# Performance work log

Measured on AMD Instinct MI355X. Metric: run time of the kernel, lower is better.

Reference implementation:

```python
import jax, jax.numpy as jnp
import numpy as np

RADIUS = 0.2
NSAMPLE = 32


def setup_inputs() -> dict:
    key = jax.random.key(0)
    k1, k2 = jax.random.split(key)
    B, N = 8, 4096
    xyz = jax.random.uniform(k1, (B, N, 3), dtype=jnp.float32)
    xyz_new = jax.random.uniform(k2, (B, N, 3), dtype=jnp.float32)  # ignored by forward, kept for signature fidelity
    return {"xyz": xyz, "xyz_new": xyz_new}


def _ball_query(radius, nsample, xyz, new_xyz):
    # xyz: [B, N, 3] source points; new_xyz: [B, M, 3] query centers.
    # Returns idx: [B, M, nsample] int32, matching pointnet2 CUDA ball_query:
    # first `nsample` indices j (in increasing j order) with ||q - p_j||^2 < r^2;
    # unused slots are filled with the first valid index.
    B, N, _ = xyz.shape
    sq_src = jnp.sum(xyz * xyz, axis=-1)          # [B, N]
    sq_q = jnp.sum(new_xyz * new_xyz, axis=-1)    # [B, M]
    # d2[b, m, n] = ||q_m - p_n||^2
    d2 = sq_q[:, :, None] + sq_src[:, None, :] - 2.0 * jnp.einsum(
        "bmc,bnc->bmn", new_xyz, xyz)             # [B, M, N]
    mask = d2 < (radius * radius)                 # [B, M, N] bool
    # key = index j when within radius, else sentinel N (sorts to the end)
    idx_range = jnp.arange(N, dtype=jnp.int32)
    keys = jnp.where(mask, idx_range[None, None, :], jnp.int32(N))
    sorted_keys = jnp.sort(keys, axis=-1)[..., :nsample]  # [B, M, nsample]
    first = sorted_keys[..., 0:1]                 # first valid index (pad value)
    idx = jnp.where(sorted_keys < N, sorted_keys, first)
    return idx.astype(jnp.int32)


def reference(xyz, xyz_new):
    # Faithful to the module: ball_query(radius, nsample, xyz, xyz) — xyz_new unused.
    return _ball_query(RADIUS, NSAMPLE, xyz, xyz)
```

## Files before the change

### kernel.cpp

```cpp
#include <hip/hip_runtime.h>
#include <cstdint>


#define BQ_N   4096
#define BQ_B   8
#define BQ_NS  32
#define BQ_R2  0.04f

__device__ __forceinline__ float sq_plain(float x, float y, float z) {
    float r, t;
    asm("v_mul_f32 %0, %2, %2\n\t"
        "v_mul_f32 %1, %3, %3\n\t"
        "v_add_f32 %0, %0, %1\n\t"
        "v_mul_f32 %1, %4, %4\n\t"
        "v_add_f32 %0, %0, %1"
        : "=&v"(r), "=&v"(t)
        : "v"(x), "v"(y), "v"(z));
    return r;
}

__device__ __forceinline__ float d2_mixed(float qx, float qy, float qz, float sqq,
                                          float sx, float sy, float sz, float sqs) {
    float r, t;
    asm("v_mul_f32 %0, %2, %5\n\t"
        "v_fma_f32 %0, %3, %6, %0\n\t"
        "v_fma_f32 %0, %4, %7, %0\n\t"
        "v_add_f32 %0, %0, %0\n\t"
        "v_add_f32 %1, %8, %9\n\t"
        "v_sub_f32 %0, %1, %0"
        : "=&v"(r), "=&v"(t)
        : "v"(qx), "v"(qy), "v"(qz), "v"(sx), "v"(sy), "v"(sz),
          "v"(sqq), "v"(sqs));
    return r;
}

__device__ __forceinline__ void emit_query(int* orow, int lane, uint64_t word) {
    const int cnt = __popcll(word);
    int incl = cnt;
    #pragma unroll
    for (int off = 1; off < 64; off <<= 1) {
        const int t = __shfl_up(incl, off);
        if (lane >= off) incl += t;
    }
    const int pre   = incl - cnt;
    const int total = __shfl(incl, 63);

    int first;
    const uint64_t nz = __ballot(word != 0ull);
    if (nz == 0ull) {
        first = BQ_N;
    } else {
        const int fl = __builtin_ctzll(nz);
        const uint64_t fw = __shfl(word, fl);
        first = (fl << 6) + __builtin_ctzll(fw);
    }

    uint64_t w = word;
    int pos = pre;
    while (w != 0ull && pos < BQ_NS) {
        const int bit = __builtin_ctzll(w);
        orow[pos] = (lane << 6) + bit;
        w &= (w - 1);
        ++pos;
    }
    if (lane >= total && lane < BQ_NS) orow[lane] = first;
}

__global__ __launch_bounds__(512, 4)
void ball_query_kernel(const float* __restrict__ xyz, int* __restrict__ out)
{
    __shared__ float4 pts[BQ_N];

    const int b     = blockIdx.x >> 6;
    const int qbase = (blockIdx.x & 63) << 6;
    const float* __restrict__ src = xyz + (size_t)b * BQ_N * 3;
    const int lane = threadIdx.x & 63;
    const int wid  = threadIdx.x >> 6;
    int* __restrict__ outb = out + (size_t)(b * BQ_N) * BQ_NS;

    for (int j = threadIdx.x; j < BQ_N; j += 512) {
        const float x = src[3 * j + 0];
        const float y = src[3 * j + 1];
        const float z = src[3 * j + 2];
        pts[j] = make_float4(x, y, z, sq_plain(x, y, z));
    }
    __syncthreads();

    float4 Q[8];
    #pragma unroll
    for (int j = 0; j < 8; ++j) Q[j] = pts[qbase + (wid << 3) + j];

    uint64_t W[8] = {0, 0, 0, 0, 0, 0, 0, 0};
    int      F[8] = {0, 0, 0, 0, 0, 0, 0, 0};
    unsigned active = 0xFFu;

    #pragma unroll 1
    for (int c = 0; c < 16 && active; ++c) {
        #pragma unroll
        for (int u = 0; u < 4; ++u) {
            const int k = (c << 2) + u;
            const float4 s = pts[(k << 6) + lane];
            #pragma unroll
            for (int i = 0; i < 8; ++i) {
                if (active & (1u << i)) {
                    const float d2 = d2_mixed(Q[i].x, Q[i].y, Q[i].z, Q[i].w,
                                              s.x, s.y, s.z, s.w);
                    const uint64_t bal = __ballot(d2 < BQ_R2);
                    if (lane == k) W[i] = bal;
                    F[i] += (int)__popcll(bal);
                }
            }
        }
        #pragma unroll
        for (int i = 0; i < 8; ++i)
            if (F[i] >= BQ_NS) active &= ~(1u << i);
    }

    #pragma unroll 1
    for (int j = 0; j < 8; ++j) {
        const int m = qbase + (wid << 3) + j;
        emit_query(outb + (size_t)m * BQ_NS, lane, W[j]);
    }
}

extern "C" void kernel_launch(void* const* d_in, const int* in_sizes, int n_in,
                              void* d_out, int out_size, void* d_ws, size_t ws_size,
                              hipStream_t stream)
{
    const float* xyz = (const float*)d_in[0];
    int* out = (int*)d_out;
    hipLaunchKernelGGL(ball_query_kernel, dim3(BQ_B * 64), dim3(512), 0, stream,
                       xyz, out);
}
```

Baseline: 85.85 us.

## Halve shared-memory staging, split queries across more blocks, keep queries in SGPRs

Each block now handles 32 queries instead of 64 and stages source points in two 2048-point halves in LDS, launching twice as many blocks with a higher occupancy hint. Query coordinates are loaded directly from global memory and broadcast to scalar registers via readfirstlane, so the distance asm takes scalar operands and frees VGPRs. The aim is more resident waves per CU and lower register pressure. In exchange, total global point loads double across blocks and the second half is always loaded even when all queries already found enough neighbours, plus an extra barrier.

```diff
diff --git a/kernel.cpp b/kernel.cpp
--- a/kernel.cpp
+++ b/kernel.cpp
@@ -2,10 +2,11 @@
 #include <cstdint>
 
 
-#define BQ_N   4096
-#define BQ_B   8
-#define BQ_NS  32
-#define BQ_R2  0.04f
+#define BQ_N    4096
+#define BQ_HALF 2048
+#define BQ_B    8
+#define BQ_NS   32
+#define BQ_R2   0.04f
 
 __device__ __forceinline__ float sq_plain(float x, float y, float z) {
     float r, t;
@@ -19,8 +20,10 @@
     return r;
 }
 
-__device__ __forceinline__ float d2_mixed(float qx, float qy, float qz, float sqq,
-                                          float sx, float sy, float sz, float sqs) {
+__device__ __forceinline__ float d2_mixed_s(float qx, float qy, float qz,
+                                            float sqq,
+                                            float sx, float sy, float sz,
+                                            float sqs) {
     float r, t;
     asm("v_mul_f32 %0, %2, %5\n\t"
         "v_fma_f32 %0, %3, %6, %0\n\t"
@@ -29,9 +32,13 @@
         "v_add_f32 %1, %8, %9\n\t"
         "v_sub_f32 %0, %1, %0"
         : "=&v"(r), "=&v"(t)
-        : "v"(qx), "v"(qy), "v"(qz), "v"(sx), "v"(sy), "v"(sz),
-          "v"(sqq), "v"(sqs));
+        : "s"(qx), "s"(qy), "s"(qz), "v"(sx), "v"(sy), "v"(sz),
+          "s"(sqq), "v"(sqs));
     return r;
+}
+
+__device__ __forceinline__ float rfl(float v) {
+    return __int_as_float(__builtin_amdgcn_readfirstlane(__float_as_int(v)));
 }
 
 __device__ __forceinline__ void emit_query(int* orow, int lane, uint64_t word) {
@@ -66,19 +73,30 @@
     if (lane >= total && lane < BQ_NS) orow[lane] = first;
 }
 
-__global__ __launch_bounds__(512, 4)
+__global__ __launch_bounds__(512, 8)
 void ball_query_kernel(const float* __restrict__ xyz, int* __restrict__ out)
 {
-    __shared__ float4 pts[BQ_N];
+    __shared__ float4 pts[BQ_HALF];
 
-    const int b     = blockIdx.x >> 6;
-    const int qbase = (blockIdx.x & 63) << 6;
+    const int b     = blockIdx.x >> 7;
+    const int qbase = (blockIdx.x & 127) << 5;
     const float* __restrict__ src = xyz + (size_t)b * BQ_N * 3;
     const int lane = threadIdx.x & 63;
     const int wid  = threadIdx.x >> 6;
     int* __restrict__ outb = out + (size_t)(b * BQ_N) * BQ_NS;
 
-    for (int j = threadIdx.x; j < BQ_N; j += 512) {
+    float qx[4], qy[4], qz[4], qw[4];
+    #pragma unroll
+    for (int j = 0; j < 4; ++j) {
+        const int m = qbase + (wid << 2) + j;
+        const float x = src[3 * m + 0];
+        const float y = src[3 * m + 1];
+        const float z = src[3 * m + 2];
+        const float w = sq_plain(x, y, z);
+        qx[j] = rfl(x); qy[j] = rfl(y); qz[j] = rfl(z); qw[j] = rfl(w);
+    }
+
+    for (int j = threadIdx.x; j < BQ_HALF; j += 512) {
         const float x = src[3 * j + 0];
         const float y = src[3 * j + 1];
         const float z = src[3 * j + 2];
@@ -86,25 +104,21 @@
     }
     __syncthreads();
 
-    float4 Q[8];
-    #pragma unroll
-    for (int j = 0; j < 8; ++j) Q[j] = pts[qbase + (wid << 3) + j];
-
-    uint64_t W[8] = {0, 0, 0, 0, 0, 0, 0, 0};
-    int      F[8] = {0, 0, 0, 0, 0, 0, 0, 0};
-    unsigned active = 0xFFu;
+    uint64_t W[4] = {0, 0, 0, 0};
+    int      F[4] = {0, 0, 0, 0};
+    unsigned active = 0xFu;
 
     #pragma unroll 1
-    for (int c = 0; c < 16 && active; ++c) {
+    for (int c = 0; c < 8 && active; ++c) {
         #pragma unroll
         for (int u = 0; u < 4; ++u) {
             const int k = (c << 2) + u;
             const float4 s = pts[(k << 6) + lane];
             #pragma unroll
-            for (int i = 0; i < 8; ++i) {
+            for (int i = 0; i < 4; ++i) {
                 if (active & (1u << i)) {
-                    const float d2 = d2_mixed(Q[i].x, Q[i].y, Q[i].z, Q[i].w,
-                                              s.x, s.y, s.z, s.w);
+                    const float d2 = d2_mixed_s(qx[i], qy[i], qz[i], qw[i],
+                                                s.x, s.y, s.z, s.w);
                     const uint64_t bal = __ballot(d2 < BQ_R2);
                     if (lane == k) W[i] = bal;
                     F[i] += (int)__popcll(bal);
@@ -112,13 +126,46 @@
             }
         }
         #pragma unroll
-        for (int i = 0; i < 8; ++i)
+        for (int i = 0; i < 4; ++i)
+            if (F[i] >= BQ_NS) active &= ~(1u << i);
+    }
+
+    __syncthreads();
+    for (int j = threadIdx.x; j < BQ_HALF; j += 512) {
+        const int g = BQ_HALF + j;
+        const float x = src[3 * g + 0];
+        const float y = src[3 * g + 1];
+        const float z = src[3 * g + 2];
+        pts[j] = make_float4(x, y, z, sq_plain(x, y, z));
+    }
+    __syncthreads();
+
+    #pragma unroll 1
+    for (int c = 0; c < 8 && active; ++c) {
+        #pragma unroll
+        for (int u = 0; u < 4; ++u) {
+            const int k  = (c << 2) + u;
+            const int k2 = 32 + k;
+            const float4 s = pts[(k << 6) + lane];
+            #pragma unroll
+            for (int i = 0; i < 4; ++i) {
+                if (active & (1u << i)) {
+                    const float d2 = d2_mixed_s(qx[i], qy[i], qz[i], qw[i],
+                                                s.x, s.y, s.z, s.w);
+                    const uint64_t bal = __ballot(d2 < BQ_R2);
+                    if (lane == k2) W[i] = bal;
+                    F[i] += (int)__popcll(bal);
+                }
+            }
+        }
+        #pragma unroll
+        for (int i = 0; i < 4; ++i)
             if (F[i] >= BQ_NS) active &= ~(1u << i);
     }
 
     #pragma unroll 1
-    for (int j = 0; j < 8; ++j) {
-        const int m = qbase + (wid << 3) + j;
+    for (int j = 0; j < 4; ++j) {
+        const int m = qbase + (wid << 2) + j;
         emit_query(outb + (size_t)m * BQ_NS, lane, W[j]);
     }
 }
@@ -129,6 +176,6 @@
 {
     const float* xyz = (const float*)d_in[0];
     int* out = (int*)d_out;
-    hipLaunchKernelGGL(ball_query_kernel, dim3(BQ_B * 64), dim3(512), 0, stream,
+    hipLaunchKernelGGL(ball_query_kernel, dim3(1024), dim3(512), 0, stream,
                        xyz, out);
 }
```

After: 84.30 us. About the same (-1.8%).

## Split each query group's source scan across two waves and keep queries in SGPRs

Applied to the files above, without the earlier changes.

Each group of 8 queries is now handled by a pair of waves, each scanning one half of the source points. The two halves' bitmasks are combined through shared memory before emission. Query coordinates are loaded from global memory and broadcast into scalar registers with readfirstlane, so the distance math takes SGPR operands. Grid size doubles with 32 queries per block and launch bounds are raised to allow more occupancy. In exchange, per-query early masking is replaced by an all-done break, so finished queries may still be computed, and a second barrier is added.

```diff
diff --git a/kernel.cpp b/kernel.cpp
--- a/kernel.cpp
+++ b/kernel.cpp
@@ -19,8 +19,10 @@
     return r;
 }
 
-__device__ __forceinline__ float d2_mixed(float qx, float qy, float qz, float sqq,
-                                          float sx, float sy, float sz, float sqs) {
+__device__ __forceinline__ float d2_mixed_s(float qx, float qy, float qz,
+                                            float sqq,
+                                            float sx, float sy, float sz,
+                                            float sqs) {
     float r, t;
     asm("v_mul_f32 %0, %2, %5\n\t"
         "v_fma_f32 %0, %3, %6, %0\n\t"
@@ -29,9 +31,13 @@
         "v_add_f32 %1, %8, %9\n\t"
         "v_sub_f32 %0, %1, %0"
         : "=&v"(r), "=&v"(t)
-        : "v"(qx), "v"(qy), "v"(qz), "v"(sx), "v"(sy), "v"(sz),
-          "v"(sqq), "v"(sqs));
+        : "s"(qx), "s"(qy), "s"(qz), "v"(sx), "v"(sy), "v"(sz),
+          "s"(sqq), "v"(sqs));
     return r;
+}
+
+__device__ __forceinline__ float rfl(float v) {
+    return __int_as_float(__builtin_amdgcn_readfirstlane(__float_as_int(v)));
 }
 
 __device__ __forceinline__ void emit_query(int* orow, int lane, uint64_t word) {
@@ -66,17 +72,31 @@
     if (lane >= total && lane < BQ_NS) orow[lane] = first;
 }
 
-__global__ __launch_bounds__(512, 4)
+__global__ __launch_bounds__(512, 8)
 void ball_query_kernel(const float* __restrict__ xyz, int* __restrict__ out)
 {
     __shared__ float4 pts[BQ_N];
+    __shared__ unsigned long long xw[4][8][32];
 
-    const int b     = blockIdx.x >> 6;
-    const int qbase = (blockIdx.x & 63) << 6;
+    const int b     = blockIdx.x >> 7;
+    const int qbase = (blockIdx.x & 127) << 5;
     const float* __restrict__ src = xyz + (size_t)b * BQ_N * 3;
     const int lane = threadIdx.x & 63;
     const int wid  = threadIdx.x >> 6;
+    const int pair = wid >> 1;
+    const int half = wid & 1;
     int* __restrict__ outb = out + (size_t)(b * BQ_N) * BQ_NS;
+
+    float qx[8], qy[8], qz[8], qw[8];
+    #pragma unroll
+    for (int j = 0; j < 8; ++j) {
+        const int m = qbase + (pair << 3) + j;
+        const float x = src[3 * m + 0];
+        const float y = src[3 * m + 1];
+        const float z = src[3 * m + 2];
+        const float w = sq_plain(x, y, z);
+        qx[j] = rfl(x); qy[j] = rfl(y); qz[j] = rfl(z); qw[j] = rfl(w);
+    }
 
     for (int j = threadIdx.x; j < BQ_N; j += 512) {
         const float x = src[3 * j + 0];
@@ -86,40 +106,47 @@
     }
     __syncthreads();
 
-    float4 Q[8];
-    #pragma unroll
-    for (int j = 0; j < 8; ++j) Q[j] = pts[qbase + (wid << 3) + j];
-
     uint64_t W[8] = {0, 0, 0, 0, 0, 0, 0, 0};
     int      F[8] = {0, 0, 0, 0, 0, 0, 0, 0};
-    unsigned active = 0xFFu;
 
+    const int kbase = half << 5;
     #pragma unroll 1
-    for (int c = 0; c < 16 && active; ++c) {
+    for (int c = 0; c < 16; ++c) {
         #pragma unroll
-        for (int u = 0; u < 4; ++u) {
-            const int k = (c << 2) + u;
+        for (int u = 0; u < 2; ++u) {
+            const int k = kbase + (c << 1) + u;
             const float4 s = pts[(k << 6) + lane];
             #pragma unroll
-            for (int i = 0; i < 8; ++i) {
-                if (active & (1u << i)) {
-                    const float d2 = d2_mixed(Q[i].x, Q[i].y, Q[i].z, Q[i].w,
-                                              s.x, s.y, s.z, s.w);
-                    const uint64_t bal = __ballot(d2 < BQ_R2);
-                    if (lane == k) W[i] = bal;
-                    F[i] += (int)__popcll(bal);
-                }
+            for (int j = 0; j < 8; ++j) {
+                const float d2 = d2_mixed_s(qx[j], qy[j], qz[j], qw[j],
+                                            s.x, s.y, s.z, s.w);
+                const uint64_t bal = __ballot(d2 < BQ_R2);
+                if (lane == k) W[j] = bal;
+                F[j] += (int)__popcll(bal);
             }
         }
+        bool all_done = true;
         #pragma unroll
-        for (int i = 0; i < 8; ++i)
-            if (F[i] >= BQ_NS) active &= ~(1u << i);
+        for (int j = 0; j < 8; ++j) all_done = all_done && (F[j] >= BQ_NS);
+        if (all_done) break;
     }
 
-    #pragma unroll 1
-    for (int j = 0; j < 8; ++j) {
-        const int m = qbase + (wid << 3) + j;
-        emit_query(outb + (size_t)m * BQ_NS, lane, W[j]);
+    if (half == 1) {
+        #pragma unroll
+        for (int j = 0; j < 8; ++j) {
+            if (lane >= 32) xw[pair][j][lane - 32] = W[j];
+        }
+    }
+    __syncthreads();
+
+    if (half == 0) {
+        #pragma unroll 1
+        for (int j = 0; j < 8; ++j) {
+            uint64_t word = W[j];
+            if (lane >= 32) word = xw[pair][j][lane - 32];
+            const int m = qbase + (pair << 3) + j;
+            emit_query(outb + (size_t)m * BQ_NS, lane, word);
+        }
     }
 }
 
@@ -129,6 +156,6 @@
 {
     const float* xyz = (const float*)d_in[0];
     int* out = (int*)d_out;
-    hipLaunchKernelGGL(ball_query_kernel, dim3(BQ_B * 64), dim3(512), 0, stream,
+    hipLaunchKernelGGL(ball_query_kernel, dim3(1024), dim3(512), 0, stream,
                        xyz, out);
 }
```

Result: slower. 119.8 us (+39.6%).
